# Performance work log

Measured on AMD Instinct MI355X. Metric: run time of the kernel, lower is better.

The kernel has to match this reference:

```python
import jax, jax.numpy as jnp
import numpy as np

ALPHA = 0.2          # LeakyReLU slope
NEG_BIG = -9e15      # mask value from the torch code
LN_EPS = 1e-5        # torch LayerNorm default eps
GAT_SCALE = 1.0


def _layer_norm(x, g, b):
    mu = x.mean(-1, keepdims=True)
    var = ((x - mu) ** 2).mean(-1, keepdims=True)
    return (x - mu) * jax.lax.rsqrt(var + LN_EPS) * g + b


def _gat_layer(h, adj, W, a, concat):
    # h: [B,N,Fin], adj: [N,N] weighted, W: [Fin,Fout], a: [2*Fout,1]
    Wh = jnp.einsum('bnf,fo->bno', h, W)                 # [B,N,Fout]
    Fo = W.shape[1]
    a_i, a_j = a[:Fo, 0], a[Fo:, 0]
    # e[b,i,j] = leakyrelu(Wh[b,i].a_i + Wh[b,j].a_j)  (== cat([Wh_i,Wh_j]) @ a)
    e = jax.nn.leaky_relu(
        (Wh @ a_i)[:, :, None] + (Wh @ a_j)[:, None, :], ALPHA)  # [B,N,N]
    att = jnp.where(adj[None, :, :] > 0, e, NEG_BIG)
    att = jax.nn.softmax(att, axis=2)
    att = att * adj[None, :, :]
    att = att / (att.sum(axis=2, keepdims=True) + 1e-8)
    h_prime = jnp.einsum('bij,bjo->bio', att, Wh)        # [B,N,Fout]
    return jax.nn.elu(h_prime) if concat else h_prime


def setup_inputs() -> dict:
    B, N, H, ID = 1024, 128, 64, 8
    GIN = 1 + ID  # node_feat_dim = 0
    key = jax.random.key(0)
    ks = jax.random.split(key, 20)
    # sparse weighted adjacency with self-loops
    w = jax.random.uniform(ks[0], (N, N))
    m = (jax.random.uniform(ks[1], (N, N)) < 0.3).astype(jnp.float32)
    adj = w * m + jnp.eye(N, dtype=jnp.float32)
    sc = lambda k, s: jax.random.normal(k, s, jnp.float32) * 0.1
    return {
        'c_values': jax.random.normal(ks[2], (B, N), jnp.float32),
        'adj': adj,
        'agent_emb': sc(ks[3], (N, ID)),
        'W1': sc(ks[4], (GIN, H)), 'a1': sc(ks[5], (2 * H, 1)),
        'W2': sc(ks[6], (H, H)),   'a2': sc(ks[7], (2 * H, 1)),
        'ln1_g': jnp.ones((H,)), 'ln1_b': jnp.zeros((H,)),
        'ln2_g': jnp.ones((H,)), 'ln2_b': jnp.zeros((H,)),
        'head_gat_w': sc(ks[8], (H, 1)), 'head_gat_b': jnp.zeros((1,)),
        'mlp1_w': sc(ks[9], (N, H)),  'mlp1_b': jnp.zeros((H,)),
        'mlp2_w': sc(ks[10], (H, H)), 'mlp2_b': jnp.zeros((H,)),
        'head_mlp_w': sc(ks[11], (H, 1)), 'head_mlp_b': jnp.zeros((1,)),
        'gate1_w': sc(ks[12], (N, H)), 'gate1_b': jnp.zeros((H,)),
        'gate2_w': sc(ks[13], (H, 1)), 'gate2_b': jnp.full((1,), -5.0),
    }


def reference(c_values, adj, agent_emb, W1, a1, W2, a2,
              ln1_g, ln1_b, ln2_g, ln2_b, head_gat_w, head_gat_b,
              mlp1_w, mlp1_b, mlp2_w, mlp2_b, head_mlp_w, head_mlp_b,
              gate1_w, gate1_b, gate2_w, gate2_b):
    B, N = c_values.shape
    # node features: [c_value, agent_id_embedding]
    id_feat = jnp.broadcast_to(agent_emb[None], (B, N, agent_emb.shape[1]))
    x_g = jnp.concatenate([c_values[..., None], id_feat], axis=-1)  # [B,N,9]
    h1 = _gat_layer(x_g, adj, W1, a1, concat=True)
    h1 = _layer_norm(h1, ln1_g, ln1_b)
    h2 = _gat_layer(h1, adj, W2, a2, concat=False)
    h = jax.nn.relu(h2 + h1)
    h = _layer_norm(h, ln2_g, ln2_b)
    q_gat = h.mean(axis=1) @ head_gat_w + head_gat_b                # [B,1]
    x_m = jax.nn.relu(c_values @ mlp1_w + mlp1_b)
    x_m = jax.nn.relu(x_m @ mlp2_w + mlp2_b)
    q_mlp = x_m @ head_mlp_w + head_mlp_b                           # [B,1]
    gate = jax.nn.sigmoid(
        jax.nn.relu(c_values @ gate1_w + gate1_b) @ gate2_w + gate2_b)
    return q_mlp + gate * GAT_SCALE * q_gat
```

## Files before the change

kernel.cpp:

```cpp
#include <hip/hip_runtime.h>
#include <hip/hip_bf16.h>

typedef unsigned short u16;
typedef unsigned int u32;
typedef short v8s __attribute__((ext_vector_type(8)));
typedef float v4f __attribute__((ext_vector_type(4)));

__device__ __forceinline__ float bflo(u32 d){union{u32 i;float f;}u;u.i=d<<16;return u.f;}
__device__ __forceinline__ float bfhi(u32 d){union{u32 i;float f;}u;u.i=d&0xffff0000u;return u.f;}
__device__ __forceinline__ u32 cvtpk(float a, float b){
    __hip_bfloat162 h = __float22bfloat162_rn(make_float2(a, b));
    u32 r; __builtin_memcpy(&r, &h, sizeof(r)); return r;
}
__device__ __forceinline__ v8s pack8(const float* w){
    union { uint4 u; v8s v; } c;
    c.u.x = cvtpk(w[0],w[1]); c.u.y = cvtpk(w[2],w[3]);
    c.u.z = cvtpk(w[4],w[5]); c.u.w = cvtpk(w[6],w[7]);
    return c.v;
}

__device__ __forceinline__ void flash_att(
    int wv, int l15, int q4,
    const float* __restrict__ ADJ,
    const float* __restrict__ sEi, const float* __restrict__ sFi,
    const float* __restrict__ sEj, const float* __restrict__ sFj,
    const u16* __restrict__ sWhT,
    v4f acc[2][4], v4f accD[2])
{
    const int r0 = 16*wv + l15, r1 = r0 + 64;
    const float Ei0 = sEi[r0], Fi0 = sFi[r0];
    const float Ei1 = sEi[r1], Fi1 = sFi[r1];
    const v8s ONES = {16256,16256,16256,16256,16256,16256,16256,16256};
    #pragma unroll
    for (int s = 0; s < 2; ++s) {
        accD[s] = (v4f){0.f,0.f,0.f,0.f};
        #pragma unroll
        for (int ct = 0; ct < 4; ++ct) acc[s][ct] = (v4f){0.f,0.f,0.f,0.f};
    }

    for (int ks = 0; ks < 4; ++ks) {
        const int ko = ks*32 + q4*8;
        float w0[8], w1[8];
        #pragma unroll
        for (int half = 0; half < 2; ++half) {
            float4 E4 = *(const float4*)(sEj + ko + 4*half);
            float4 F4 = *(const float4*)(sFj + ko + 4*half);
            float4 a0 = *(const float4*)(ADJ + r0*128 + ko + 4*half);
            float4 a1 = *(const float4*)(ADJ + r1*128 + ko + 4*half);
            float Ev[4] = {E4.x,E4.y,E4.z,E4.w};
            float Fv[4] = {F4.x,F4.y,F4.z,F4.w};
            float av0[4] = {a0.x,a0.y,a0.z,a0.w};
            float av1[4] = {a1.x,a1.y,a1.z,a1.w};
            #pragma unroll
            for (int k = 0; k < 4; ++k) {
                w0[half*4 + k] = fmaxf(Ei0*Ev[k], Fi0*Fv[k]) * av0[k];
                w1[half*4 + k] = fmaxf(Ei1*Ev[k], Fi1*Fv[k]) * av1[k];
            }
        }
        v8s A0 = pack8(w0), A1 = pack8(w1);
        accD[0] = __builtin_amdgcn_mfma_f32_16x16x32_bf16(A0, ONES, accD[0], 0,0,0);
        accD[1] = __builtin_amdgcn_mfma_f32_16x16x32_bf16(A1, ONES, accD[1], 0,0,0);
        #pragma unroll
        for (int ct = 0; ct < 4; ++ct) {
            v8s B = *(const v8s*)(sWhT + (16*ct + l15)*136 + ko);
            acc[0][ct] = __builtin_amdgcn_mfma_f32_16x16x32_bf16(A0, B, acc[0][ct], 0,0,0);
            acc[1][ct] = __builtin_amdgcn_mfma_f32_16x16x32_bf16(A1, B, acc[1][ct], 0,0,0);
        }
    }
}

__global__ __launch_bounds__(256, 4) void graphmixer_kernel(
    const float* __restrict__ C,
    const float* __restrict__ ADJ,
    const float* __restrict__ EMB,
    const float* __restrict__ W1,
    const float* __restrict__ A1,
    const float* __restrict__ W2,
    const float* __restrict__ A2,
    const float* __restrict__ LN1G, const float* __restrict__ LN1B,
    const float* __restrict__ LN2G, const float* __restrict__ LN2B,
    const float* __restrict__ HGW,  const float* __restrict__ HGB,
    const float* __restrict__ MLP1W, const float* __restrict__ MLP1B,
    const float* __restrict__ MLP2W, const float* __restrict__ MLP2B,
    const float* __restrict__ HMW,  const float* __restrict__ HMB,
    const float* __restrict__ G1W,  const float* __restrict__ G1B,
    const float* __restrict__ G2W,  const float* __restrict__ G2B,
    float* __restrict__ OUT)
{
    const int b = blockIdx.x, t = threadIdx.x;
    const int lane = t & 63, wv = t >> 6;
    const int l15 = lane & 15, q4 = lane >> 4;

    __shared__ __align__(16) unsigned char smem[40096];
    u16*   sWhT = (u16*)(smem);
    u16*   sH1  = (u16*)(smem + 17408);
    float* sEi  = (float*)(smem + 35840);
    float* sFi  = (float*)(smem + 36352);
    float* sEj  = (float*)(smem + 36864);
    float* sFj  = (float*)(smem + 37376);
    float* colp = (float*)(smem + 37888);
    float* sScr = (float*)(smem + 38912);
    float* v2i  = (float*)(smem + 39456);
    float* v2j  = (float*)(smem + 39712);
    float* v1i  = (float*)(smem + 39968);
    float* v1j  = (float*)(smem + 40032);
    float* sEmb = (float*)(smem + 17408);
    float* sC   = (float*)(smem + 21504);

    const float* Cb = C + b*128;

    if (wv == 0) {
        #pragma unroll
        for (int q = 0; q < 4; ++q)
            ((float4*)sEmb)[lane + 64*q] = ((const float4*)EMB)[lane + 64*q];
        if (lane < 32) ((float4*)sC)[lane] = ((const float4*)Cb)[lane];
        if (lane >= 32 && lane < 41) {
            int f = lane - 32; float a0 = 0.f, a1 = 0.f;
            for (int q = 0; q < 16; q += 2) {
                float4 w = *(const float4*)(W1 + f*64 + q*4);
                float4 x = *(const float4*)(A1 + q*4);
                a0 += w.x*x.x + w.y*x.y + w.z*x.z + w.w*x.w;
                float4 w2 = *(const float4*)(W1 + f*64 + (q+1)*4);
                float4 x2 = *(const float4*)(A1 + (q+1)*4);
                a1 += w2.x*x2.x + w2.y*x2.y + w2.z*x2.z + w2.w*x2.w;
            }
            v1i[f] = a0 + a1;
        } else if (lane >= 48 && lane < 57) {
            int f = lane - 48; float a0 = 0.f, a1 = 0.f;
            for (int q = 0; q < 16; q += 2) {
                float4 w = *(const float4*)(W1 + f*64 + q*4);
                float4 x = *(const float4*)(A1 + 64 + q*4);
                a0 += w.x*x.x + w.y*x.y + w.z*x.z + w.w*x.w;
                float4 w2 = *(const float4*)(W1 + f*64 + (q+1)*4);
                float4 x2 = *(const float4*)(A1 + 64 + (q+1)*4);
                a1 += w2.x*x2.x + w2.y*x2.y + w2.z*x2.z + w2.w*x2.w;
            }
            v1j[f] = a0 + a1;
        }
    } else if (wv == 3) {
        float ai0 = 0.f, ai1 = 0.f, aj0 = 0.f, aj1 = 0.f;
        for (int q = 0; q < 16; ++q) {
            float4 w  = *(const float4*)(W2 + lane*64 + q*4);
            float4 xi = *(const float4*)(A2 + q*4);
            float4 xj = *(const float4*)(A2 + 64 + q*4);
            ai0 += w.x*xi.x + w.y*xi.y; ai1 += w.z*xi.z + w.w*xi.w;
            aj0 += w.x*xj.x + w.y*xj.y; aj1 += w.z*xj.z + w.w*xj.w;
        }
        v2i[lane] = ai0 + ai1; v2j[lane] = aj0 + aj1;
    } else if (wv == 1) {
        float a0 = 0.f, a1 = 0.f, a2v = 0.f, a3 = 0.f;
        for (int k = 0; k < 128; k += 4) {
            float4 c4 = *(const float4*)(Cb + k);
            a0  += c4.x*MLP1W[k*64+lane];
            a1  += c4.y*MLP1W[(k+1)*64+lane];
            a2v += c4.z*MLP1W[(k+2)*64+lane];
            a3  += c4.w*MLP1W[(k+3)*64+lane];
        }
        sScr[lane] = fmaxf(a0+a1+a2v+a3 + MLP1B[lane], 0.f);
        float b0 = 0.f, b1 = 0.f, b2 = 0.f, b3 = 0.f;
        for (int k = 0; k < 64; k += 4) {
            b0 += sScr[k]  *MLP2W[k*64 + lane];
            b1 += sScr[k+1]*MLP2W[(k+1)*64 + lane];
            b2 += sScr[k+2]*MLP2W[(k+2)*64 + lane];
            b3 += sScr[k+3]*MLP2W[(k+3)*64 + lane];
        }
        float x2 = fmaxf(b0+b1+b2+b3 + MLP2B[lane], 0.f);
        float p1 = x2 * HMW[lane];
        #pragma unroll
        for (int off = 32; off >= 1; off >>= 1) p1 += __shfl_down(p1, off);
        if (lane == 0) sScr[128] = p1 + HMB[0];
    } else {
        float a0 = 0.f, a1 = 0.f, a2v = 0.f, a3 = 0.f;
        for (int k = 0; k < 128; k += 4) {
            float4 c4 = *(const float4*)(Cb + k);
            a0  += c4.x*G1W[k*64+lane];
            a1  += c4.y*G1W[(k+1)*64+lane];
            a2v += c4.z*G1W[(k+2)*64+lane];
            a3  += c4.w*G1W[(k+3)*64+lane];
        }
        float g1 = fmaxf(a0+a1+a2v+a3 + G1B[lane], 0.f);
        float p2 = g1 * G2W[lane];
        #pragma unroll
        for (int off = 32; off >= 1; off >>= 1) p2 += __shfl_down(p2, off);
        if (lane == 0) sScr[129] = 1.f / (1.f + __expf(-(p2 + G2B[0])));
    }
    __syncthreads();

    {
        const int o = lane, cc = wv;
        float w1f[9];
        #pragma unroll
        for (int f = 0; f < 9; ++f) w1f[f] = W1[f*64 + o];
        float whv[32];
        for (int i = 0; i < 32; ++i) {
            const int ig = cc*32 + i;
            float a = sC[ig] * w1f[0];
            float4 e0 = *(const float4*)(sEmb + ig*8);
            float4 e1 = *(const float4*)(sEmb + ig*8 + 4);
            a += e0.x*w1f[1] + e0.y*w1f[2] + e0.z*w1f[3] + e0.w*w1f[4];
            a += e1.x*w1f[5] + e1.y*w1f[6] + e1.z*w1f[7] + e1.w*w1f[8];
            whv[i] = a;
        }
        u32 p[16];
        #pragma unroll
        for (int q = 0; q < 16; ++q) p[q] = cvtpk(whv[2*q], whv[2*q+1]);
        uint4* dst = (uint4*)(sWhT + o*136 + cc*32);
        dst[0] = ((uint4*)p)[0]; dst[1] = ((uint4*)p)[1];
        dst[2] = ((uint4*)p)[2]; dst[3] = ((uint4*)p)[3];
    }
    if (t < 128) {
        float c = sC[t];
        float4 e0 = *(const float4*)(sEmb + t*8);
        float4 e1 = *(const float4*)(sEmb + t*8 + 4);
        float ei = c*v1i[0] + e0.x*v1i[1]+e0.y*v1i[2]+e0.z*v1i[3]+e0.w*v1i[4]
                            + e1.x*v1i[5]+e1.y*v1i[6]+e1.z*v1i[7]+e1.w*v1i[8];
        float ej = c*v1j[0] + e0.x*v1j[1]+e0.y*v1j[2]+e0.z*v1j[3]+e0.w*v1j[4]
                            + e1.x*v1j[5]+e1.y*v1j[6]+e1.z*v1j[7]+e1.w*v1j[8];
        sEi[t] = __expf(ei); sFi[t] = __expf(0.2f*ei);
        sEj[t] = __expf(ej); sFj[t] = __expf(0.2f*ej);
    }
    __syncthreads();

    u32 h1p[2][4][2];

    {
        v4f acc[2][4]; v4f accD[2];
        flash_att(wv, l15, q4, ADJ, sEi, sFi, sEj, sFj, sWhT, acc, accD);

        float g4[4], b4[4];
        #pragma unroll
        for (int ct = 0; ct < 4; ++ct) { g4[ct] = LN1G[16*ct + l15]; b4[ct] = LN1B[16*ct + l15]; }
        #pragma unroll
        for (int s = 0; s < 2; ++s) {
            const int rbase = 16*(wv + 4*s) + 4*q4;
            #pragma unroll
            for (int reg = 0; reg < 4; ++reg) {
                const int row = rbase + reg;
                const float rd = 1.f / accD[s][reg];
                float x[4], s1 = 0.f, s2 = 0.f;
                #pragma unroll
                for (int ct = 0; ct < 4; ++ct) {
                    float v = acc[s][ct][reg] * rd;
                    v = (v > 0.f) ? v : (__expf(v) - 1.f);
                    x[ct] = v; s1 += v; s2 += v*v;
                }
                s1 += __shfl_xor(s1, 1); s2 += __shfl_xor(s2, 1);
                s1 += __shfl_xor(s1, 2); s2 += __shfl_xor(s2, 2);
                s1 += __shfl_xor(s1, 4); s2 += __shfl_xor(s2, 4);
                s1 += __shfl_xor(s1, 8); s2 += __shfl_xor(s2, 8);
                const float mean = s1 * (1.f/64.f);
                const float var  = s2 * (1.f/64.f) - mean*mean;
                const float rstd = rsqrtf(var + 1e-5f);
                float h[4];
                #pragma unroll
                for (int ct = 0; ct < 4; ++ct)
                    h[ct] = (x[ct] - mean) * rstd * g4[ct] + b4[ct];
                const u32 p01 = cvtpk(h[0], h[1]);
                const u32 p23 = cvtpk(h[2], h[3]);
                h1p[s][reg][0] = p01; h1p[s][reg][1] = p23;
                sH1[row*72 +      l15] = (u16)(p01 & 0xffffu);
                sH1[row*72 + 16 + l15] = (u16)(p01 >> 16);
                sH1[row*72 + 32 + l15] = (u16)(p23 & 0xffffu);
                sH1[row*72 + 48 + l15] = (u16)(p23 >> 16);
            }
        }
    }
    __syncthreads();

    if (t < 128) {
        float ei = 0.f, ej = 0.f;
        const u16* hrow = sH1 + t*72;
        for (int q = 0; q < 16; ++q) {
            uint2 d = *(const uint2*)(hrow + q*4);
            float h0 = bflo(d.x), h1v = bfhi(d.x), h2 = bflo(d.y), h3 = bfhi(d.y);
            ei += h0*v2i[q*4+0] + h1v*v2i[q*4+1] + h2*v2i[q*4+2] + h3*v2i[q*4+3];
            ej += h0*v2j[q*4+0] + h1v*v2j[q*4+1] + h2*v2j[q*4+2] + h3*v2j[q*4+3];
        }
        sEi[t] = __expf(ei); sFi[t] = __expf(0.2f*ei);
        sEj[t] = __expf(ej); sFj[t] = __expf(0.2f*ej);
    }
    {
        v4f acc2[2][4];
        #pragma unroll
        for (int s = 0; s < 2; ++s)
            #pragma unroll
            for (int ct = 0; ct < 4; ++ct) acc2[s][ct] = (v4f){0.f,0.f,0.f,0.f};
        #pragma unroll
        for (int ks = 0; ks < 2; ++ks) {
            const int kb = ks*32 + q4*8;
            v8s Bf[4];
            #pragma unroll
            for (int ct = 0; ct < 4; ++ct) {
                const float* wp = W2 + kb*64 + 16*ct + l15;
                float w8[8];
                #pragma unroll
                for (int j = 0; j < 8; ++j) w8[j] = wp[j*64];
                Bf[ct] = pack8(w8);
            }
            #pragma unroll
            for (int s = 0; s < 2; ++s) {
                v8s A = *(const v8s*)(sH1 + (16*(wv+4*s) + l15)*72 + kb);
                #pragma unroll
                for (int ct = 0; ct < 4; ++ct)
                    acc2[s][ct] = __builtin_amdgcn_mfma_f32_16x16x32_bf16(A, Bf[ct], acc2[s][ct], 0,0,0);
            }
        }
        #pragma unroll
        for (int s = 0; s < 2; ++s) {
            const int rb = 16*(wv+4*s) + 4*q4;
            #pragma unroll
            for (int ct = 0; ct < 4; ++ct) {
                const int col = 16*ct + l15;
                uint2 p;
                p.x = cvtpk(acc2[s][ct][0], acc2[s][ct][1]);
                p.y = cvtpk(acc2[s][ct][2], acc2[s][ct][3]);
                *(uint2*)(sWhT + col*136 + rb) = p;
            }
        }
    }
    __syncthreads();

    {
        v4f acc[2][4]; v4f accD[2];
        flash_att(wv, l15, q4, ADJ, sEi, sFi, sEj, sFj, sWhT, acc, accD);

        float g4[4], b4[4], colsum[4];
        #pragma unroll
        for (int ct = 0; ct < 4; ++ct) {
            g4[ct] = LN2G[16*ct + l15]; b4[ct] = LN2B[16*ct + l15]; colsum[ct] = 0.f;
        }
        #pragma unroll
        for (int s = 0; s < 2; ++s) {
            #pragma unroll
            for (int reg = 0; reg < 4; ++reg) {
                const float rd = 1.f / accD[s][reg];
                float x[4], s1 = 0.f, s2 = 0.f;
                #pragma unroll
                for (int ct = 0; ct < 4; ++ct) {
                    const u32 pw = h1p[s][reg][ct >> 1];
                    const float h1v = (ct & 1) ? bfhi(pw) : bflo(pw);
                    float v = fmaxf(acc[s][ct][reg] * rd + h1v, 0.f);
                    x[ct] = v; s1 += v; s2 += v*v;
                }
                s1 += __shfl_xor(s1, 1); s2 += __shfl_xor(s2, 1);
                s1 += __shfl_xor(s1, 2); s2 += __shfl_xor(s2, 2);
                s1 += __shfl_xor(s1, 4); s2 += __shfl_xor(s2, 4);
                s1 += __shfl_xor(s1, 8); s2 += __shfl_xor(s2, 8);
                const float mean = s1 * (1.f/64.f);
                const float var  = s2 * (1.f/64.f) - mean*mean;
                const float rstd = rsqrtf(var + 1e-5f);
                #pragma unroll
                for (int ct = 0; ct < 4; ++ct)
                    colsum[ct] += (x[ct] - mean) * rstd * g4[ct] + b4[ct];
            }
        }
        #pragma unroll
        for (int ct = 0; ct < 4; ++ct) {
            colsum[ct] += __shfl_xor(colsum[ct], 16);
            colsum[ct] += __shfl_xor(colsum[ct], 32);
        }
        if (lane < 16) {
            #pragma unroll
            for (int ct = 0; ct < 4; ++ct) colp[wv*64 + ct*16 + lane] = colsum[ct];
        }
    }
    __syncthreads();

    if (wv == 0) {
        float s = colp[lane] + colp[64 + lane] + colp[128 + lane] + colp[192 + lane];
        float p = s * (1.f/128.f) * HGW[lane];
        #pragma unroll
        for (int off = 32; off >= 1; off >>= 1) p += __shfl_down(p, off);
        if (lane == 0) OUT[b] = sScr[128] + sScr[129] * (p + HGB[0]);
    }
}

extern "C" void kernel_launch(void* const* d_in, const int* in_sizes, int n_in,
                              void* d_out, int out_size, void* d_ws, size_t ws_size,
                              hipStream_t stream) {
    (void)n_in; (void)out_size; (void)d_ws; (void)ws_size;
    const float* C     = (const float*)d_in[0];
    const float* ADJ   = (const float*)d_in[1];
    const float* EMB   = (const float*)d_in[2];
    const float* W1    = (const float*)d_in[3];
    const float* A1    = (const float*)d_in[4];
    const float* W2    = (const float*)d_in[5];
    const float* A2    = (const float*)d_in[6];
    const float* LN1G  = (const float*)d_in[7];
    const float* LN1B  = (const float*)d_in[8];
    const float* LN2G  = (const float*)d_in[9];
    const float* LN2B  = (const float*)d_in[10];
    const float* HGW   = (const float*)d_in[11];
    const float* HGB   = (const float*)d_in[12];
    const float* MLP1W = (const float*)d_in[13];
    const float* MLP1B = (const float*)d_in[14];
    const float* MLP2W = (const float*)d_in[15];
    const float* MLP2B = (const float*)d_in[16];
    const float* HMW   = (const float*)d_in[17];
    const float* HMB   = (const float*)d_in[18];
    const float* G1W   = (const float*)d_in[19];
    const float* G1B   = (const float*)d_in[20];
    const float* G2W   = (const float*)d_in[21];
    const float* G2B   = (const float*)d_in[22];

    const int B = in_sizes[0] / 128;

    graphmixer_kernel<<<dim3(B), dim3(256), 0, stream>>>(
        C, ADJ, EMB, W1, A1, W2, A2, LN1G, LN1B, LN2G, LN2B,
        HGW, HGB, MLP1W, MLP1B, MLP2W, MLP2B, HMW, HMB,
        G1W, G1B, G2W, G2B, (float*)d_out);
}
```

Before: 131.1 us.

## Transpose MFMA operands so each lane owns a row, fusing LN and attention logits

Swaps the A/B operands of the attention MFMAs so the output accumulator is transposed: each lane holds four consecutive feature columns of one node row. This lets the LayerNorm reductions use two cross-half shuffles instead of four per register. It also fuses the layer-2 attention logit dot products into the LN1 epilogue, removing a separate serial 128-thread pass over shared memory. The LN2 epilogue folds the head weight directly into a per-lane scalar, which simplifies the final reduction. The row-sum denominator is now read from a single accumulator slot, which relies on the transposed ONES product giving identical values across the slots.

```diff
diff --git a/kernel.cpp b/kernel.cpp
--- a/kernel.cpp
+++ b/kernel.cpp
@@ -58,13 +58,13 @@
             }
         }
         v8s A0 = pack8(w0), A1 = pack8(w1);
-        accD[0] = __builtin_amdgcn_mfma_f32_16x16x32_bf16(A0, ONES, accD[0], 0,0,0);
-        accD[1] = __builtin_amdgcn_mfma_f32_16x16x32_bf16(A1, ONES, accD[1], 0,0,0);
+        accD[0] = __builtin_amdgcn_mfma_f32_16x16x32_bf16(ONES, A0, accD[0], 0,0,0);
+        accD[1] = __builtin_amdgcn_mfma_f32_16x16x32_bf16(ONES, A1, accD[1], 0,0,0);
         #pragma unroll
         for (int ct = 0; ct < 4; ++ct) {
-            v8s B = *(const v8s*)(sWhT + (16*ct + l15)*136 + ko);
-            acc[0][ct] = __builtin_amdgcn_mfma_f32_16x16x32_bf16(A0, B, acc[0][ct], 0,0,0);
-            acc[1][ct] = __builtin_amdgcn_mfma_f32_16x16x32_bf16(A1, B, acc[1][ct], 0,0,0);
+            v8s Wt = *(const v8s*)(sWhT + (16*ct + l15)*136 + ko);
+            acc[0][ct] = __builtin_amdgcn_mfma_f32_16x16x32_bf16(Wt, A0, acc[0][ct], 0,0,0);
+            acc[1][ct] = __builtin_amdgcn_mfma_f32_16x16x32_bf16(Wt, A1, acc[1][ct], 0,0,0);
         }
     }
 }
@@ -221,64 +221,72 @@
     }
     __syncthreads();
 
-    u32 h1p[2][4][2];
+    uint2 h1p[2][4];
+    float e2i[2], e2j[2];
 
     {
         v4f acc[2][4]; v4f accD[2];
         flash_att(wv, l15, q4, ADJ, sEi, sFi, sEj, sFj, sWhT, acc, accD);
 
-        float g4[4], b4[4];
-        #pragma unroll
-        for (int ct = 0; ct < 4; ++ct) { g4[ct] = LN1G[16*ct + l15]; b4[ct] = LN1B[16*ct + l15]; }
+        float4 g4[4], b4[4], vi4[4], vj4[4];
+        #pragma unroll
+        for (int ct = 0; ct < 4; ++ct) {
+            g4[ct] = *(const float4*)(LN1G + 16*ct + 4*q4);
+            b4[ct] = *(const float4*)(LN1B + 16*ct + 4*q4);
+            vi4[ct] = *(const float4*)(v2i + 16*ct + 4*q4);
+            vj4[ct] = *(const float4*)(v2j + 16*ct + 4*q4);
+        }
         #pragma unroll
         for (int s = 0; s < 2; ++s) {
-            const int rbase = 16*(wv + 4*s) + 4*q4;
-            #pragma unroll
-            for (int reg = 0; reg < 4; ++reg) {
-                const int row = rbase + reg;
-                const float rd = 1.f / accD[s][reg];
-                float x[4], s1 = 0.f, s2 = 0.f;
+            const int row = 16*wv + l15 + 64*s;
+            const float rd = 1.f / accD[s][0];
+            float x[4][4]; float s1 = 0.f, s2 = 0.f;
+            #pragma unroll
+            for (int ct = 0; ct < 4; ++ct) {
                 #pragma unroll
-                for (int ct = 0; ct < 4; ++ct) {
+                for (int reg = 0; reg < 4; ++reg) {
                     float v = acc[s][ct][reg] * rd;
                     v = (v > 0.f) ? v : (__expf(v) - 1.f);
-                    x[ct] = v; s1 += v; s2 += v*v;
+                    x[ct][reg] = v;
                 }
-                s1 += __shfl_xor(s1, 1); s2 += __shfl_xor(s2, 1);
-                s1 += __shfl_xor(s1, 2); s2 += __shfl_xor(s2, 2);
-                s1 += __shfl_xor(s1, 4); s2 += __shfl_xor(s2, 4);
-                s1 += __shfl_xor(s1, 8); s2 += __shfl_xor(s2, 8);
-                const float mean = s1 * (1.f/64.f);
-                const float var  = s2 * (1.f/64.f) - mean*mean;
-                const float rstd = rsqrtf(var + 1e-5f);
-                float h[4];
-                #pragma unroll
-                for (int ct = 0; ct < 4; ++ct)
-                    h[ct] = (x[ct] - mean) * rstd * g4[ct] + b4[ct];
-                const u32 p01 = cvtpk(h[0], h[1]);
-                const u32 p23 = cvtpk(h[2], h[3]);
-                h1p[s][reg][0] = p01; h1p[s][reg][1] = p23;
-                sH1[row*72 +      l15] = (u16)(p01 & 0xffffu);
-                sH1[row*72 + 16 + l15] = (u16)(p01 >> 16);
-                sH1[row*72 + 32 + l15] = (u16)(p23 & 0xffffu);
-                sH1[row*72 + 48 + l15] = (u16)(p23 >> 16);
-            }
+                s1 += (x[ct][0]+x[ct][1]) + (x[ct][2]+x[ct][3]);
+                s2 += (x[ct][0]*x[ct][0]+x[ct][1]*x[ct][1])
+                    + (x[ct][2]*x[ct][2]+x[ct][3]*x[ct][3]);
+            }
+            s1 += __shfl_xor(s1, 16); s2 += __shfl_xor(s2, 16);
+            s1 += __shfl_xor(s1, 32); s2 += __shfl_xor(s2, 32);
+            const float mean = s1 * (1.f/64.f);
+            const float var  = s2 * (1.f/64.f) - mean*mean;
+            const float rstd = rsqrtf(var + 1e-5f);
+            float ei = 0.f, ej = 0.f;
+            #pragma unroll
+            for (int ct = 0; ct < 4; ++ct) {
+                float h0 = (x[ct][0] - mean) * rstd * g4[ct].x + b4[ct].x;
+                float h1 = (x[ct][1] - mean) * rstd * g4[ct].y + b4[ct].y;
+                float h2 = (x[ct][2] - mean) * rstd * g4[ct].z + b4[ct].z;
+                float h3 = (x[ct][3] - mean) * rstd * g4[ct].w + b4[ct].w;
+                uint2 pw; pw.x = cvtpk(h0, h1); pw.y = cvtpk(h2, h3);
+                h1p[s][ct] = pw;
+                *(uint2*)(sH1 + row*72 + 16*ct + 4*q4) = pw;
+                ei += h0*vi4[ct].x + h1*vi4[ct].y + h2*vi4[ct].z + h3*vi4[ct].w;
+                ej += h0*vj4[ct].x + h1*vj4[ct].y + h2*vj4[ct].z + h3*vj4[ct].w;
+            }
+            ei += __shfl_xor(ei, 16); ei += __shfl_xor(ei, 32);
+            ej += __shfl_xor(ej, 16); ej += __shfl_xor(ej, 32);
+            e2i[s] = ei; e2j[s] = ej;
         }
     }
     __syncthreads();
 
-    if (t < 128) {
-        float ei = 0.f, ej = 0.f;
-        const u16* hrow = sH1 + t*72;
-        for (int q = 0; q < 16; ++q) {
-            uint2 d = *(const uint2*)(hrow + q*4);
-            float h0 = bflo(d.x), h1v = bfhi(d.x), h2 = bflo(d.y), h3 = bfhi(d.y);
-            ei += h0*v2i[q*4+0] + h1v*v2i[q*4+1] + h2*v2i[q*4+2] + h3*v2i[q*4+3];
-            ej += h0*v2j[q*4+0] + h1v*v2j[q*4+1] + h2*v2j[q*4+2] + h3*v2j[q*4+3];
-        }
-        sEi[t] = __expf(ei); sFi[t] = __expf(0.2f*ei);
-        sEj[t] = __expf(ej); sFj[t] = __expf(0.2f*ej);
-    }
+    if (q4 == 0) {
+        #pragma unroll
+        for (int s = 0; s < 2; ++s) {
+            const int row = 16*wv + l15 + 64*s;
+            sEi[row] = __expf(e2i[s]); sFi[row] = __expf(0.2f*e2i[s]);
+            sEj[row] = __expf(e2j[s]); sFj[row] = __expf(0.2f*e2j[s]);
+        }
+    }
+
     {
         v4f acc2[2][4];
         #pragma unroll
@@ -324,54 +332,53 @@
         v4f acc[2][4]; v4f accD[2];
         flash_att(wv, l15, q4, ADJ, sEi, sFi, sEj, sFj, sWhT, acc, accD);
 
-        float g4[4], b4[4], colsum[4];
+        float4 g4[4], b4[4], hg4[4];
         #pragma unroll
         for (int ct = 0; ct < 4; ++ct) {
-            g4[ct] = LN2G[16*ct + l15]; b4[ct] = LN2B[16*ct + l15]; colsum[ct] = 0.f;
-        }
+            g4[ct] = *(const float4*)(LN2G + 16*ct + 4*q4);
+            b4[ct] = *(const float4*)(LN2B + 16*ct + 4*q4);
+            hg4[ct] = *(const float4*)(HGW + 16*ct + 4*q4);
+        }
+        float ptot = 0.f;
         #pragma unroll
         for (int s = 0; s < 2; ++s) {
-            #pragma unroll
-            for (int reg = 0; reg < 4; ++reg) {
-                const float rd = 1.f / accD[s][reg];
-                float x[4], s1 = 0.f, s2 = 0.f;
+            const float rd = 1.f / accD[s][0];
+            float x[4][4]; float s1 = 0.f, s2 = 0.f;
+            #pragma unroll
+            for (int ct = 0; ct < 4; ++ct) {
+                const uint2 pw = h1p[s][ct];
+                const float hv[4] = {bflo(pw.x), bfhi(pw.x), bflo(pw.y), bfhi(pw.y)};
                 #pragma unroll
-                for (int ct = 0; ct < 4; ++ct) {
-                    const u32 pw = h1p[s][reg][ct >> 1];
-                    const float h1v = (ct & 1) ? bfhi(pw) : bflo(pw);
-                    float v = fmaxf(acc[s][ct][reg] * rd + h1v, 0.f);
-                    x[ct] = v; s1 += v; s2 += v*v;
-                }
-                s1 += __shfl_xor(s1, 1); s2 += __shfl_xor(s2, 1);
-                s1 += __shfl_xor(s1, 2); s2 += __shfl_xor(s2, 2);
-                s1 += __shfl_xor(s1, 4); s2 += __shfl_xor(s2, 4);
-                s1 += __shfl_xor(s1, 8); s2 += __shfl_xor(s2, 8);
-                const float mean = s1 * (1.f/64.f);
-                const float var  = s2 * (1.f/64.f) - mean*mean;
-                const float rstd = rsqrtf(var + 1e-5f);
-                #pragma unroll
-                for (int ct = 0; ct < 4; ++ct)
-                    colsum[ct] += (x[ct] - mean) * rstd * g4[ct] + b4[ct];
-            }
-        }
-        #pragma unroll
-        for (int ct = 0; ct < 4; ++ct) {
-            colsum[ct] += __shfl_xor(colsum[ct], 16);
-            colsum[ct] += __shfl_xor(colsum[ct], 32);
-        }
-        if (lane < 16) {
-            #pragma unroll
-            for (int ct = 0; ct < 4; ++ct) colp[wv*64 + ct*16 + lane] = colsum[ct];
-        }
+                for (int reg = 0; reg < 4; ++reg)
+                    x[ct][reg] = fmaxf(acc[s][ct][reg] * rd + hv[reg], 0.f);
+                s1 += (x[ct][0]+x[ct][1]) + (x[ct][2]+x[ct][3]);
+                s2 += (x[ct][0]*x[ct][0]+x[ct][1]*x[ct][1])
+                    + (x[ct][2]*x[ct][2]+x[ct][3]*x[ct][3]);
+            }
+            s1 += __shfl_xor(s1, 16); s2 += __shfl_xor(s2, 16);
+            s1 += __shfl_xor(s1, 32); s2 += __shfl_xor(s2, 32);
+            const float mean = s1 * (1.f/64.f);
+            const float var  = s2 * (1.f/64.f) - mean*mean;
+            const float rstd = rsqrtf(var + 1e-5f);
+            #pragma unroll
+            for (int ct = 0; ct < 4; ++ct) {
+                float y0 = (x[ct][0] - mean) * rstd * g4[ct].x + b4[ct].x;
+                float y1 = (x[ct][1] - mean) * rstd * g4[ct].y + b4[ct].y;
+                float y2 = (x[ct][2] - mean) * rstd * g4[ct].z + b4[ct].z;
+                float y3 = (x[ct][3] - mean) * rstd * g4[ct].w + b4[ct].w;
+                ptot += y0*hg4[ct].x + y1*hg4[ct].y + y2*hg4[ct].z + y3*hg4[ct].w;
+            }
+        }
+        ptot += __shfl_xor(ptot, 1);  ptot += __shfl_xor(ptot, 2);
+        ptot += __shfl_xor(ptot, 4);  ptot += __shfl_xor(ptot, 8);
+        ptot += __shfl_xor(ptot, 16); ptot += __shfl_xor(ptot, 32);
+        if (lane == 0) colp[wv] = ptot;
     }
     __syncthreads();
 
-    if (wv == 0) {
-        float s = colp[lane] + colp[64 + lane] + colp[128 + lane] + colp[192 + lane];
-        float p = s * (1.f/128.f) * HGW[lane];
-        #pragma unroll
-        for (int off = 32; off >= 1; off >>= 1) p += __shfl_down(p, off);
-        if (lane == 0) OUT[b] = sScr[128] + sScr[129] * (p + HGB[0]);
+    if (t == 0) {
+        float s4 = (colp[0] + colp[1]) + (colp[2] + colp[3]);
+        OUT[b] = sScr[128] + sScr[129] * (s4 * (1.f/128.f) + HGB[0]);
     }
 }
 
```

Measured after the change: 132.8 us. Within noise of the previous version (+1.3%).
